# Performance work log

Hardware: AMD Instinct MI355X
Metric: run time of the kernel (lower is better)

The kernel has to match this reference:

```python
import jax, jax.numpy as jnp
import numpy as np

S, B, DM, H, DFF = 2048, 4, 1024, 16, 4096
DK = DM // H  # 64, dv == dk
EPS = 1e-5

def layer_norm(x, g, b):
    mu = jnp.mean(x, axis=-1, keepdims=True)
    var = jnp.var(x, axis=-1, keepdims=True)
    return (x - mu) * jax.lax.rsqrt(var + EPS) * g + b

def setup_inputs() -> dict:
    key = jax.random.key(0)
    ks = jax.random.split(key, 12)
    sc = 0.02
    return {
        "X": jax.random.normal(ks[0], (S, B, DM), dtype=jnp.float32),
        # stacked per-head projections: weight [H, dk, dm], bias [H, dk]
        "WQ_w": jax.random.normal(ks[1], (H, DK, DM), dtype=jnp.float32) * sc,
        "WQ_b": jnp.zeros((H, DK), dtype=jnp.float32),
        "WK_w": jax.random.normal(ks[2], (H, DK, DM), dtype=jnp.float32) * sc,
        "WK_b": jnp.zeros((H, DK), dtype=jnp.float32),
        "WV_w": jax.random.normal(ks[3], (H, DK, DM), dtype=jnp.float32) * sc,
        "WV_b": jnp.zeros((H, DK), dtype=jnp.float32),
        "WO_w": jax.random.normal(ks[4], (DM, H * DK), dtype=jnp.float32) * sc,
        "WO_b": jnp.zeros((DM,), dtype=jnp.float32),
        "ln1_g": jnp.ones((DM,), dtype=jnp.float32),
        "ln1_b": jnp.zeros((DM,), dtype=jnp.float32),
        "W1": jax.random.normal(ks[5], (DFF, DM), dtype=jnp.float32) * sc,
        "b1": jnp.zeros((DFF,), dtype=jnp.float32),
        "W2": jax.random.normal(ks[6], (DM, DFF), dtype=jnp.float32) * sc,
        "b2": jnp.zeros((DM,), dtype=jnp.float32),
        "ln2_g": jnp.ones((DM,), dtype=jnp.float32),
        "ln2_b": jnp.zeros((DM,), dtype=jnp.float32),
    }

def reference(X, WQ_w, WQ_b, WK_w, WK_b, WV_w, WV_b, WO_w, WO_b,
              ln1_g, ln1_b, W1, b1, W2, b2, ln2_g, ln2_b):
    # --- self-attention (encoder: no causal mask, no key_mask, drop=0) ---
    # X: [S, B, DM]; per-head Q/K/V: [S, B, H, DK]
    Q = jnp.einsum('sbd,hkd->sbhk', X, WQ_w) + WQ_b
    K = jnp.einsum('sbd,hkd->sbhk', X, WK_w) + WK_b
    V = jnp.einsum('sbd,hvd->sbhv', X, WV_w) + WV_b
    scores = jnp.einsum('sbhk,lbhk->sbhl', Q, K) / jnp.sqrt(jnp.float32(DK))
    attn = jax.nn.softmax(scores, axis=-1)  # softmax over keys l
    ctx = jnp.einsum('sbhl,lbhv->sbhv', attn, V)
    # concat heads (head-major order matches torch.concat over head list)
    ctx = ctx.reshape(S, B, H * DK)
    y = ctx @ WO_w.T + WO_b
    X1 = layer_norm(y + X, ln1_g, ln1_b)
    # --- MLP (1 hidden layer, ReLU) ---
    h = jax.nn.relu(X1 @ W1.T + b1)
    m = h @ W2.T + b2
    return layer_norm(m + X1, ln2_g, ln2_b)
```

## Files before the change

kernel.cpp:

```cpp
#include <hip/hip_runtime.h>
#include <stdint.h>

typedef short bf16x8 __attribute__((ext_vector_type(8)));
typedef float f32x4 __attribute__((ext_vector_type(4)));
typedef float f32x16 __attribute__((ext_vector_type(16)));

__device__ __forceinline__ float bf2f(uint16_t u) {
    union { uint32_t i; float f; } c; c.i = ((uint32_t)u) << 16; return c.f;
}
__device__ __forceinline__ uint16_t f2bf(float f) {
    union { float f; uint32_t i; } c; c.f = f;
    uint32_t x = c.i;
    return (uint16_t)((x + 0x7fffu + ((x >> 16) & 1u)) >> 16);
}
__device__ __forceinline__ uint32_t pack2t(float lo, float hi) {
    union { float f; uint32_t u; } a, b;
    a.f = lo; b.f = hi;
    return __builtin_amdgcn_perm(b.u, a.u, 0x07060302u);
}

__device__ __forceinline__ void load_lds16(const void* g, void* lds) {
    using gp_t = const __attribute__((address_space(1))) uint32_t*;
    using lp_t = __attribute__((address_space(3))) uint32_t*;
    __builtin_amdgcn_global_load_lds(
        reinterpret_cast<gp_t>(reinterpret_cast<uintptr_t>(g)),
        reinterpret_cast<lp_t>((uint32_t)reinterpret_cast<uintptr_t>(lds)),
        16, 0, 0);
}

__global__ __launch_bounds__(256) void cvt_kernel(
    const float* __restrict__ s, uint16_t* __restrict__ d, int n)
{
    int i = (blockIdx.x * 256 + threadIdx.x) * 4;
    if (i < n) {
        float4 v = *(const float4*)(s + i);
        ushort4 o;
        o.x = f2bf(v.x); o.y = f2bf(v.y); o.z = f2bf(v.z); o.w = f2bf(v.w);
        *(ushort4*)(d + i) = o;
    }
}

__global__ __launch_bounds__(256) void cvt_w6(
    const float* __restrict__ q, const float* __restrict__ k,
    const float* __restrict__ v, const float* __restrict__ o,
    const float* __restrict__ m1, const float* __restrict__ m2,
    uint16_t* __restrict__ d)
{
    const int M = 1048576;
    size_t i = ((size_t)blockIdx.x * 256 + threadIdx.x) * 4;
    const float* s; size_t off;
    if (i < (size_t)M)          { s = q;  off = i; }
    else if (i < 2ull * M)      { s = k;  off = i - M; }
    else if (i < 3ull * M)      { s = v;  off = i - 2ull * M; }
    else if (i < 4ull * M)      { s = o;  off = i - 3ull * M; }
    else if (i < 8ull * M)      { s = m1; off = i - 4ull * M; }
    else                        { s = m2; off = i - 8ull * M; }
    float4 x = *(const float4*)(s + off);
    ushort4 u;
    u.x = f2bf(x.x); u.y = f2bf(x.y); u.z = f2bf(x.z); u.w = f2bf(x.w);
    *(ushort4*)(d + i) = u;
}

__global__ __launch_bounds__(256) void cvt_bias6(
    const float* __restrict__ q, const float* __restrict__ k,
    const float* __restrict__ v, const float* __restrict__ o,
    const float* __restrict__ m1, const float* __restrict__ m2,
    uint16_t* __restrict__ d)
{
    int i = (blockIdx.x * 256 + threadIdx.x) * 4;
    if (i >= 9216) return;
    const float* s; int off;
    if (i < 1024)      { s = q;  off = i; }
    else if (i < 2048) { s = k;  off = i - 1024; }
    else if (i < 3072) { s = v;  off = i - 2048; }
    else if (i < 4096) { s = o;  off = i - 3072; }
    else if (i < 8192) { s = m1; off = i - 4096; }
    else               { s = m2; off = i - 8192; }
    float4 x = *(const float4*)(s + off);
    ushort4 u;
    u.x = f2bf(x.x); u.y = f2bf(x.y); u.z = f2bf(x.z); u.w = f2bf(x.w);
    *(ushort4*)(d + i) = u;
}

template<int MODE>
__global__ __launch_bounds__(256) void gemm_bt(
    const uint16_t* __restrict__ A, const uint16_t* __restrict__ B,
    const uint16_t* __restrict__ bias, uint16_t* __restrict__ C,
    int K, int N, int relu)
{
    __shared__ uint16_t sA[128 * 64];
    __shared__ uint16_t sB[128 * 64];
    const int tid = threadIdx.x;
    const int w = tid >> 6, ln = tid & 63;
    const int m = ln & 15, q = ln >> 4;
    const int wr = w >> 1, wc = w & 1;
    const int tm = blockIdx.y * 128, tn = blockIdx.x * 128;

    f32x4 zero = {0.f, 0.f, 0.f, 0.f};
    f32x4 acc[4][4];
#pragma unroll
    for (int i = 0; i < 4; ++i)
#pragma unroll
        for (int j = 0; j < 4; ++j) acc[i][j] = zero;

    const int sr = tid >> 3;
    const int sc_ = tid & 7;
    const int g = sc_ ^ (sr & 7);

    for (int k0 = 0; k0 < K; k0 += 64) {
        __syncthreads();
#pragma unroll
        for (int i = 0; i < 4; ++i) {
            int r = i * 32 + sr;
            load_lds16(A + (size_t)(tm + r) * K + k0 + g * 8, &sA[(i * 32 + w * 8) * 64]);
            load_lds16(B + (size_t)(tn + r) * K + k0 + g * 8, &sB[(i * 32 + w * 8) * 64]);
        }
        __syncthreads();
#pragma unroll
        for (int kk = 0; kk < 2; ++kk) {
            bf16x8 af[4], bfr[4];
            const int s = (kk * 4 + q) ^ (m & 7);
#pragma unroll
            for (int rt = 0; rt < 4; ++rt) {
                int R = wr * 64 + rt * 16 + m;
                af[rt] = *(const bf16x8*)&sA[R * 64 + s * 8];
            }
#pragma unroll
            for (int ct = 0; ct < 4; ++ct) {
                int R = wc * 64 + ct * 16 + m;
                bfr[ct] = *(const bf16x8*)&sB[R * 64 + s * 8];
            }
#pragma unroll
            for (int rt = 0; rt < 4; ++rt)
#pragma unroll
                for (int ct = 0; ct < 4; ++ct)
                    acc[rt][ct] = __builtin_amdgcn_mfma_f32_16x16x32_bf16(
                        af[rt], bfr[ct], acc[rt][ct], 0, 0, 0);
        }
    }

    const int sect = tn >> 10;
#pragma unroll
    for (int ct = 0; ct < 4; ++ct) {
        int col = tn + wc * 64 + ct * 16 + m;
        float bv = bf2f(bias[col]);
#pragma unroll
        for (int rt = 0; rt < 4; ++rt) {
            int rowb = tm + wr * 64 + rt * 16 + q * 4;
#pragma unroll
            for (int rg = 0; rg < 4; ++rg) {
                int t = rowb + rg;
                float v = acc[rt][ct][rg] + bv;
                if (relu) v = fmaxf(v, 0.f);
                size_t off;
                if (MODE == 0) {
                    off = (size_t)t * N + col;
                } else {
                    int c = col & 1023;
                    int bh = (t & 3) * 16 + (c >> 6);
                    if (sect == 0) {
                        off = (size_t)bh * 131072 + (t >> 2) * 64 + (c & 63);
                        v *= 0.18033688f;
                    } else if (sect == 1) {
                        off = 8388608ull + (size_t)bh * 131072 + (t >> 2) * 64 + (c & 63);
                    } else {
                        off = 16777216ull + (size_t)bh * 131072 + (size_t)(c & 63) * 2048 + (t >> 2);
                    }
                }
                C[off] = f2bf(v);
            }
        }
    }
}

__global__ __launch_bounds__(256) void attn2(
    const uint16_t* __restrict__ Qh, const uint16_t* __restrict__ Kh,
    const uint16_t* __restrict__ Vt, uint16_t* __restrict__ CTX)
{
    __shared__ uint16_t sK[64 * 64];
    __shared__ uint16_t sV[64 * 64];
    __shared__ uint16_t sP[128 * 72];

    const int tid = threadIdx.x;
    const int w = tid >> 6, ln = tid & 63;
    const int m5 = ln & 31, h5 = ln >> 5;
    const int bh = blockIdx.x, qt = blockIdx.y;
    const uint16_t* Qb = Qh + (size_t)bh * 131072;
    const uint16_t* Kb = Kh + (size_t)bh * 131072;
    const uint16_t* Vb = Vt + (size_t)bh * 131072;

    const int qrow = qt * 128 + w * 32 + m5;
    bf16x8 qf[4];
#pragma unroll
    for (int ks = 0; ks < 4; ++ks)
        qf[ks] = *(const bf16x8*)(Qb + (size_t)qrow * 64 + ks * 16 + h5 * 8);

    f32x16 Oa[2];
#pragma unroll
    for (int nb = 0; nb < 2; ++nb)
#pragma unroll
        for (int i = 0; i < 16; ++i) Oa[nb][i] = 0.f;
    float psum = 0.f;

    const int sr = tid >> 3;
    const int sc_ = tid & 7;
    const int g = sc_ ^ (sr & 7);

    for (int c = 0; c < 32; ++c) {
        __syncthreads();
        load_lds16(Kb + (size_t)(c * 64 + sr) * 64 + g * 8,        &sK[tid * 8]);
        load_lds16(Kb + (size_t)(c * 64 + sr + 32) * 64 + g * 8,   &sK[2048 + tid * 8]);
        load_lds16(Vb + (size_t)sr * 2048 + c * 64 + g * 8,        &sV[tid * 8]);
        load_lds16(Vb + (size_t)(sr + 32) * 2048 + c * 64 + g * 8, &sV[2048 + tid * 8]);
        __syncthreads();

#pragma unroll
        for (int kb = 0; kb < 2; ++kb) {
            f32x16 acc;
#pragma unroll
            for (int i = 0; i < 16; ++i) acc[i] = 0.f;
#pragma unroll
            for (int ks = 0; ks < 4; ++ks) {
                int row = kb * 32 + m5;
                int ph = (2 * ks + h5) ^ (m5 & 7);
                bf16x8 kf = *(const bf16x8*)&sK[row * 64 + ph * 8];
                acc = __builtin_amdgcn_mfma_f32_32x32x16_bf16(kf, qf[ks], acc, 0, 0, 0);
            }
#pragma unroll
            for (int a = 0; a < 4; ++a) {
                float p0 = exp2f(acc[4 * a + 0]);
                float p1 = exp2f(acc[4 * a + 1]);
                float p2 = exp2f(acc[4 * a + 2]);
                float p3 = exp2f(acc[4 * a + 3]);
                psum += (p0 + p1) + (p2 + p3);
                uint2 d;
                d.x = pack2t(p0, p1);
                d.y = pack2t(p2, p3);
                int log8 = kb * 8 + 2 * a + h5;
                int ph8 = log8 ^ (m5 & 7);
                *(uint2*)&sP[(w * 32 + m5) * 72 + ph8 * 4] = d;
            }
        }

#pragma unroll
        for (int ks = 0; ks < 4; ++ks) {
            int pr = w * 32 + m5;
            int la = 4 * ks + 2 * h5;
            uint2 lo = *(const uint2*)&sP[pr * 72 + ((la) ^ (m5 & 7)) * 4];
            uint2 hi = *(const uint2*)&sP[pr * 72 + ((la + 1) ^ (m5 & 7)) * 4];
            union { uint2 u[2]; bf16x8 v; } pu;
            pu.u[0] = lo; pu.u[1] = hi;
#pragma unroll
            for (int nb = 0; nb < 2; ++nb) {
                int vrow = nb * 32 + m5;
                int ph = (2 * ks + h5) ^ (m5 & 7);
                bf16x8 vf = *(const bf16x8*)&sV[vrow * 64 + ph * 8];
                Oa[nb] = __builtin_amdgcn_mfma_f32_32x32x16_bf16(pu.v, vf, Oa[nb], 0, 0, 0);
            }
        }
    }

    float l = psum + __shfl_xor(psum, 32);
    float linv = 1.f / l;
    float li[16];
#pragma unroll
    for (int a = 0; a < 4; ++a)
#pragma unroll
        for (int r = 0; r < 4; ++r)
            li[4 * a + r] = __shfl(linv, r + 8 * a + 4 * h5);

    const int b_ = bh >> 4, h_ = bh & 15;
#pragma unroll
    for (int nb = 0; nb < 2; ++nb)
#pragma unroll
        for (int a = 0; a < 4; ++a)
#pragma unroll
            for (int r = 0; r < 4; ++r) {
                int qr = r + 8 * a + 4 * h5;
                int s = qt * 128 + w * 32 + qr;
                int col = h_ * 64 + nb * 32 + m5;
                CTX[(size_t)(s * 4 + b_) * 1024 + col] = f2bf(Oa[nb][4 * a + r] * li[4 * a + r]);
            }
}

template<bool RES_F32, bool OUT_F32>
__global__ __launch_bounds__(256) void ln_resid(
    const uint16_t* __restrict__ Y, const void* __restrict__ Xp,
    const float* __restrict__ G, const float* __restrict__ Bv,
    void* __restrict__ Op)
{
    const int row = blockIdx.x, tid = threadIdx.x;
    const size_t base = (size_t)row * 1024 + tid * 4;
    ushort4 yv = *(const ushort4*)(Y + base);
    float x0, x1, x2, x3;
    if (RES_F32) {
        float4 xv = *(const float4*)((const float*)Xp + base);
        x0 = xv.x; x1 = xv.y; x2 = xv.z; x3 = xv.w;
    } else {
        ushort4 xv = *(const ushort4*)((const uint16_t*)Xp + base);
        x0 = bf2f(xv.x); x1 = bf2f(xv.y); x2 = bf2f(xv.z); x3 = bf2f(xv.w);
    }
    float v0 = bf2f(yv.x) + x0;
    float v1 = bf2f(yv.y) + x1;
    float v2 = bf2f(yv.z) + x2;
    float v3 = bf2f(yv.w) + x3;
    float s = v0 + v1 + v2 + v3;
    float ss = v0 * v0 + v1 * v1 + v2 * v2 + v3 * v3;
#pragma unroll
    for (int off = 32; off > 0; off >>= 1) {
        s += __shfl_down(s, off);
        ss += __shfl_down(ss, off);
    }
    __shared__ float rs[4], rss[4];
    if ((tid & 63) == 0) { rs[tid >> 6] = s; rss[tid >> 6] = ss; }
    __syncthreads();
    float S = rs[0] + rs[1] + rs[2] + rs[3];
    float SS = rss[0] + rss[1] + rss[2] + rss[3];
    const float invn = 1.f / 1024.f;
    float mu = S * invn;
    float var = SS * invn - mu * mu;
    float rstd = rsqrtf(var + 1e-5f);
    float4 gv = *(const float4*)(G + tid * 4);
    float4 bv = *(const float4*)(Bv + tid * 4);
    float o0 = (v0 - mu) * rstd * gv.x + bv.x;
    float o1 = (v1 - mu) * rstd * gv.y + bv.y;
    float o2 = (v2 - mu) * rstd * gv.z + bv.z;
    float o3 = (v3 - mu) * rstd * gv.w + bv.w;
    if (OUT_F32) {
        float4 o = {o0, o1, o2, o3};
        *(float4*)((float*)Op + base) = o;
    } else {
        ushort4 o;
        o.x = f2bf(o0); o.y = f2bf(o1); o.z = f2bf(o2); o.w = f2bf(o3);
        *(ushort4*)((uint16_t*)Op + base) = o;
    }
}

extern "C" void kernel_launch(void* const* d_in, const int* in_sizes, int n_in,
                              void* d_out, int out_size, void* d_ws, size_t ws_size,
                              hipStream_t stream)
{
    const float* X    = (const float*)d_in[0];
    const float* WQw  = (const float*)d_in[1];
    const float* WQb  = (const float*)d_in[2];
    const float* WKw  = (const float*)d_in[3];
    const float* WKb  = (const float*)d_in[4];
    const float* WVw  = (const float*)d_in[5];
    const float* WVb  = (const float*)d_in[6];
    const float* WOw  = (const float*)d_in[7];
    const float* WOb  = (const float*)d_in[8];
    const float* ln1g = (const float*)d_in[9];
    const float* ln1b = (const float*)d_in[10];
    const float* W1   = (const float*)d_in[11];
    const float* b1   = (const float*)d_in[12];
    const float* W2   = (const float*)d_in[13];
    const float* b2   = (const float*)d_in[14];
    const float* ln2g = (const float*)d_in[15];
    const float* ln2b = (const float*)d_in[16];

    uint16_t* ws = (uint16_t*)d_ws;
    const size_t E = 8192ull * 1024ull;
    const size_t MW = 1048576ull;
    uint16_t* Xb   = ws;
    uint16_t* qh   = ws + E;
    uint16_t* kh   = ws + 2 * E;
    uint16_t* vt   = ws + 3 * E;
    uint16_t* ctx  = ws + 4 * E;
    uint16_t* y    = qh;
    uint16_t* x1   = kh;
    uint16_t* m2   = vt;
    uint16_t* hbuf = ws + 5 * E;
    uint16_t* wq   = ws + 9 * E;
    uint16_t* wo   = wq + 3 * MW;
    uint16_t* w1   = wo + MW;
    uint16_t* w2   = w1 + 4 * MW;
    uint16_t* bq   = w2 + 4 * MW;
    uint16_t* bo   = bq + 3072;
    uint16_t* bb1  = bo + 1024;
    uint16_t* bb2  = bb1 + 4096;

    cvt_kernel<<<dim3(8192), dim3(256), 0, stream>>>(X, Xb, (int)E);
    cvt_w6<<<dim3(12288), dim3(256), 0, stream>>>(WQw, WKw, WVw, WOw, W1, W2, wq);
    cvt_bias6<<<dim3(9), dim3(256), 0, stream>>>(WQb, WKb, WVb, WOb, b1, b2, bq);

    dim3 blk(256);
    gemm_bt<3><<<dim3(24, 64), blk, 0, stream>>>(Xb,   wq, bq,  qh,   1024, 3072, 0);
    attn2<<<dim3(64, 16), blk, 0, stream>>>(qh, kh, vt, ctx);
    gemm_bt<0><<<dim3(8, 64),  blk, 0, stream>>>(ctx,  wo, bo,  y,    1024, 1024, 0);
    ln_resid<true, false><<<dim3(8192), blk, 0, stream>>>(y, X, ln1g, ln1b, x1);
    gemm_bt<0><<<dim3(32, 64), blk, 0, stream>>>(x1,   w1, bb1, hbuf, 1024, 4096, 1);
    gemm_bt<0><<<dim3(8, 64),  blk, 0, stream>>>(hbuf, w2, bb2, m2,   4096, 1024, 0);
    ln_resid<false, true><<<dim3(8192), blk, 0, stream>>>(m2, x1, ln2g, ln2b, d_out);
}
```

Measured before the change: 581.0 us.

## Keep attention P in registers via lane shuffles; narrow N-tile for DM-output GEMMs

```diff
diff --git a/kernel.cpp b/kernel.cpp
--- a/kernel.cpp
+++ b/kernel.cpp
@@ -4,6 +4,7 @@
 typedef short bf16x8 __attribute__((ext_vector_type(8)));
 typedef float f32x4 __attribute__((ext_vector_type(4)));
 typedef float f32x16 __attribute__((ext_vector_type(16)));
+typedef uint32_t u32x4 __attribute__((ext_vector_type(4)));
 
 __device__ __forceinline__ float bf2f(uint16_t u) {
     union { uint32_t i; float f; } c; c.i = ((uint32_t)u) << 16; return c.f;
@@ -82,26 +83,27 @@
     *(ushort4*)(d + i) = u;
 }
 
-template<int MODE>
+template<int MODE, int NT>
 __global__ __launch_bounds__(256) void gemm_bt(
     const uint16_t* __restrict__ A, const uint16_t* __restrict__ B,
     const uint16_t* __restrict__ bias, uint16_t* __restrict__ C,
     int K, int N, int relu)
 {
+    const int CT = NT / 32;
     __shared__ uint16_t sA[128 * 64];
-    __shared__ uint16_t sB[128 * 64];
+    __shared__ uint16_t sB[NT * 64];
     const int tid = threadIdx.x;
     const int w = tid >> 6, ln = tid & 63;
     const int m = ln & 15, q = ln >> 4;
     const int wr = w >> 1, wc = w & 1;
-    const int tm = blockIdx.y * 128, tn = blockIdx.x * 128;
+    const int tm = blockIdx.y * 128, tn = blockIdx.x * NT;
 
     f32x4 zero = {0.f, 0.f, 0.f, 0.f};
-    f32x4 acc[4][4];
+    f32x4 acc[4][CT];
 #pragma unroll
     for (int i = 0; i < 4; ++i)
 #pragma unroll
-        for (int j = 0; j < 4; ++j) acc[i][j] = zero;
+        for (int j = 0; j < CT; ++j) acc[i][j] = zero;
 
     const int sr = tid >> 3;
     const int sc_ = tid & 7;
@@ -113,12 +115,16 @@
         for (int i = 0; i < 4; ++i) {
             int r = i * 32 + sr;
             load_lds16(A + (size_t)(tm + r) * K + k0 + g * 8, &sA[(i * 32 + w * 8) * 64]);
+        }
+#pragma unroll
+        for (int i = 0; i < NT / 32; ++i) {
+            int r = i * 32 + sr;
             load_lds16(B + (size_t)(tn + r) * K + k0 + g * 8, &sB[(i * 32 + w * 8) * 64]);
         }
         __syncthreads();
 #pragma unroll
         for (int kk = 0; kk < 2; ++kk) {
-            bf16x8 af[4], bfr[4];
+            bf16x8 af[4], bfr[CT];
             const int s = (kk * 4 + q) ^ (m & 7);
 #pragma unroll
             for (int rt = 0; rt < 4; ++rt) {
@@ -126,14 +132,14 @@
                 af[rt] = *(const bf16x8*)&sA[R * 64 + s * 8];
             }
 #pragma unroll
-            for (int ct = 0; ct < 4; ++ct) {
-                int R = wc * 64 + ct * 16 + m;
+            for (int ct = 0; ct < CT; ++ct) {
+                int R = wc * (NT / 2) + ct * 16 + m;
                 bfr[ct] = *(const bf16x8*)&sB[R * 64 + s * 8];
             }
 #pragma unroll
             for (int rt = 0; rt < 4; ++rt)
 #pragma unroll
-                for (int ct = 0; ct < 4; ++ct)
+                for (int ct = 0; ct < CT; ++ct)
                     acc[rt][ct] = __builtin_amdgcn_mfma_f32_16x16x32_bf16(
                         af[rt], bfr[ct], acc[rt][ct], 0, 0, 0);
         }
@@ -141,8 +147,8 @@
 
     const int sect = tn >> 10;
 #pragma unroll
-    for (int ct = 0; ct < 4; ++ct) {
-        int col = tn + wc * 64 + ct * 16 + m;
+    for (int ct = 0; ct < CT; ++ct) {
+        int col = tn + wc * (NT / 2) + ct * 16 + m;
         float bv = bf2f(bias[col]);
 #pragma unroll
         for (int rt = 0; rt < 4; ++rt) {
@@ -179,7 +185,6 @@
 {
     __shared__ uint16_t sK[64 * 64];
     __shared__ uint16_t sV[64 * 64];
-    __shared__ uint16_t sP[128 * 72];
 
     const int tid = threadIdx.x;
     const int w = tid >> 6, ln = tid & 63;
@@ -226,36 +231,41 @@
                 bf16x8 kf = *(const bf16x8*)&sK[row * 64 + ph * 8];
                 acc = __builtin_amdgcn_mfma_f32_32x32x16_bf16(kf, qf[ks], acc, 0, 0, 0);
             }
-#pragma unroll
-            for (int a = 0; a < 4; ++a) {
-                float p0 = exp2f(acc[4 * a + 0]);
-                float p1 = exp2f(acc[4 * a + 1]);
-                float p2 = exp2f(acc[4 * a + 2]);
-                float p3 = exp2f(acc[4 * a + 3]);
-                psum += (p0 + p1) + (p2 + p3);
-                uint2 d;
-                d.x = pack2t(p0, p1);
-                d.y = pack2t(p2, p3);
-                int log8 = kb * 8 + 2 * a + h5;
-                int ph8 = log8 ^ (m5 & 7);
-                *(uint2*)&sP[(w * 32 + m5) * 72 + ph8 * 4] = d;
-            }
-        }
-
-#pragma unroll
-        for (int ks = 0; ks < 4; ++ks) {
-            int pr = w * 32 + m5;
-            int la = 4 * ks + 2 * h5;
-            uint2 lo = *(const uint2*)&sP[pr * 72 + ((la) ^ (m5 & 7)) * 4];
-            uint2 hi = *(const uint2*)&sP[pr * 72 + ((la + 1) ^ (m5 & 7)) * 4];
-            union { uint2 u[2]; bf16x8 v; } pu;
-            pu.u[0] = lo; pu.u[1] = hi;
-#pragma unroll
-            for (int nb = 0; nb < 2; ++nb) {
-                int vrow = nb * 32 + m5;
-                int ph = (2 * ks + h5) ^ (m5 & 7);
-                bf16x8 vf = *(const bf16x8*)&sV[vrow * 64 + ph * 8];
-                Oa[nb] = __builtin_amdgcn_mfma_f32_32x32x16_bf16(pu.v, vf, Oa[nb], 0, 0, 0);
+            float p[16];
+#pragma unroll
+            for (int i = 0; i < 16; ++i) p[i] = exp2f(acc[i]);
+#pragma unroll
+            for (int i = 0; i < 16; i += 4)
+                psum += (p[i] + p[i + 1]) + (p[i + 2] + p[i + 3]);
+            uint32_t u[8], x[8];
+#pragma unroll
+            for (int t = 0; t < 4; ++t) {
+                u[2 * t]     = pack2t(p[4 * t],     p[4 * t + 1]);
+                u[2 * t + 1] = pack2t(p[4 * t + 2], p[4 * t + 3]);
+            }
+#pragma unroll
+            for (int j = 0; j < 8; ++j)
+                x[j] = (uint32_t)__shfl_xor((int)u[j], 32);
+            union { u32x4 q; bf16x8 v; } f0, f1;
+            f0.q[0] = h5 ? x[2] : u[0];
+            f0.q[1] = h5 ? x[3] : u[1];
+            f0.q[2] = h5 ? u[2] : x[0];
+            f0.q[3] = h5 ? u[3] : x[1];
+            f1.q[0] = h5 ? x[6] : u[4];
+            f1.q[1] = h5 ? x[7] : u[5];
+            f1.q[2] = h5 ? u[6] : x[4];
+            f1.q[3] = h5 ? u[7] : x[5];
+#pragma unroll
+            for (int ks2 = 0; ks2 < 2; ++ks2) {
+                int ks = kb * 2 + ks2;
+                bf16x8 pf = ks2 ? f1.v : f0.v;
+#pragma unroll
+                for (int nb = 0; nb < 2; ++nb) {
+                    int vrow = nb * 32 + m5;
+                    int ph = (2 * ks + h5) ^ (m5 & 7);
+                    bf16x8 vf = *(const bf16x8*)&sV[vrow * 64 + ph * 8];
+                    Oa[nb] = __builtin_amdgcn_mfma_f32_32x32x16_bf16(pf, vf, Oa[nb], 0, 0, 0);
+                }
             }
         }
     }
@@ -384,11 +394,11 @@
     cvt_bias6<<<dim3(9), dim3(256), 0, stream>>>(WQb, WKb, WVb, WOb, b1, b2, bq);
 
     dim3 blk(256);
-    gemm_bt<3><<<dim3(24, 64), blk, 0, stream>>>(Xb,   wq, bq,  qh,   1024, 3072, 0);
+    gemm_bt<3, 128><<<dim3(24, 64), blk, 0, stream>>>(Xb,   wq, bq,  qh,   1024, 3072, 0);
     attn2<<<dim3(64, 16), blk, 0, stream>>>(qh, kh, vt, ctx);
-    gemm_bt<0><<<dim3(8, 64),  blk, 0, stream>>>(ctx,  wo, bo,  y,    1024, 1024, 0);
+    gemm_bt<0, 64><<<dim3(16, 64),  blk, 0, stream>>>(ctx,  wo, bo,  y,    1024, 1024, 0);
     ln_resid<true, false><<<dim3(8192), blk, 0, stream>>>(y, X, ln1g, ln1b, x1);
-    gemm_bt<0><<<dim3(32, 64), blk, 0, stream>>>(x1,   w1, bb1, hbuf, 1024, 4096, 1);
-    gemm_bt<0><<<dim3(8, 64),  blk, 0, stream>>>(hbuf, w2, bb2, m2,   4096, 1024, 0);
+    gemm_bt<0, 128><<<dim3(32, 64), blk, 0, stream>>>(x1,   w1, bb1, hbuf, 1024, 4096, 1);
+    gemm_bt<0, 64><<<dim3(16, 64),  blk, 0, stream>>>(hbuf, w2, bb2, m2,   4096, 1024, 0);
     ln_resid<false, true><<<dim3(8192), blk, 0, stream>>>(m2, x1, ln2g, ln2b, d_out);
 }
```

After: 580.6 us. About the same (-0.1%).
